# Kernel tuning notes

Measured on AMD Instinct MI355X. Metric: run time of the kernel, lower is better.

Reference implementation:

```python
import jax, jax.numpy as jnp
import numpy as np

B = 32768

def _lin(x, w, b):
    return x @ w.T + b

def setup_inputs() -> dict:
    key = jax.random.key(0)
    ks = iter(jax.random.split(key, 40))
    def rn(shape, s=0.05):
        return jax.random.normal(next(ks), shape, dtype=jnp.float32) * s
    inp = {
        'img_feat': jax.random.normal(next(ks), (B, 256), dtype=jnp.float32),
        'instruction_idx': jax.random.randint(next(ks), (B, 1), 0, 4),
        '_hx': jax.random.normal(next(ks), (B, 256), dtype=jnp.float32),
        '_cx': jax.random.normal(next(ks), (B, 256), dtype=jnp.float32),
        'query': jax.random.normal(next(ks), (B, 256), dtype=jnp.float32),
        # parameters
        'emb': rn((4, 25), 1.0),
        'w_ta': rn((256, 25)), 'b_ta': rn((256,)),
        'w_ih': rn((1024, 512)), 'w_hh': rn((1024, 256)),
        'b_ih': rn((1024,)), 'b_hh': rn((1024,)),
        'w_q': rn((256, 256)), 'b_q': rn((256,)),
        'w_k': rn((256, 256)), 'b_k': rn((256,)),
        'w_ba': rn((512, 512)), 'b_ba': rn((512,)),
        'w_at': rn((256, 512)), 'b_at': rn((256,)),
        'w_p1': rn((128, 256)), 'b_p1': rn((128,)),
        'w_p2': rn((64, 128)), 'b_p2': rn((64,)),
        'w_p': rn((3, 64)), 'b_p': rn((3,)),
        'w_v1': rn((64, 256)), 'b_v1': rn((64,)),
        'w_v2': rn((32, 64)), 'b_v2': rn((32,)),
        'w_v': rn((1, 32)), 'b_v': rn((1,)),
    }
    return inp

def reference(img_feat, instruction_idx, _hx, _cx, query,
              emb, w_ta, b_ta, w_ih, w_hh, b_ih, b_hh,
              w_q, b_q, w_k, b_k, w_ba, b_ba, w_at, b_at,
              w_p1, b_p1, w_p2, b_p2, w_p, b_p,
              w_v1, b_v1, w_v2, b_v2, w_v, b_v):
    # embedding lookup [B,1,25] -> [B,25]
    we = emb[instruction_idx].reshape(instruction_idx.shape[0], -1)
    gated_att = jax.nn.sigmoid(_lin(we, w_ta, b_ta))          # [B,256]
    gated_fusion = img_feat * gated_att                        # [B,256]
    lstm_input = jnp.concatenate([gated_fusion, gated_att], 1) # [B,512]
    # LSTMCell (PyTorch gate order: i, f, g, o)
    gates = lstm_input @ w_ih.T + b_ih + _hx @ w_hh.T + b_hh   # [B,1024]
    i, f, g, o = jnp.split(gates, 4, axis=1)
    cx = jax.nn.sigmoid(f) * _cx + jax.nn.sigmoid(i) * jnp.tanh(g)
    hx = jax.nn.sigmoid(o) * jnp.tanh(cx)
    mlp_input = jnp.concatenate([gated_fusion, hx], 1)         # [B,512]
    mlp_attn = jax.nn.relu(_lin(mlp_input, w_ba, b_ba))        # [B,512]
    key_, val = jnp.split(mlp_attn, 2, axis=1)                 # [B,256] each
    w_q_out = jax.nn.relu(_lin(query, w_q, b_q))
    w_k_out = jax.nn.relu(_lin(key_, w_k, b_k))
    u_t = jnp.tanh(w_q_out + w_k_out)
    attention_vector = u_t * val
    attn_weight = jnp.concatenate([attention_vector, hx], 1)   # [B,512]
    attn_weight = jax.nn.relu(_lin(attn_weight, w_at, b_at))   # [B,256]
    pol = jax.nn.relu(_lin(attn_weight, w_p1, b_p1))
    pol = jax.nn.relu(_lin(pol, w_p2, b_p2))
    valh = jax.nn.relu(_lin(attn_weight, w_v1, b_v1))
    valh = jax.nn.relu(_lin(valh, w_v2, b_v2))
    return (_lin(valh, w_v, b_v), _lin(pol, w_p, b_p), hx, cx)
```

## Files before the change

kernel.cpp:

```cpp
#include <hip/hip_runtime.h>

typedef unsigned short u16;
typedef __bf16 bf16x8 __attribute__((ext_vector_type(8)));
typedef float f32x4 __attribute__((ext_vector_type(4)));
typedef u16 u16x8 __attribute__((ext_vector_type(8)));
typedef u16 u16x4 __attribute__((ext_vector_type(4)));

#define TM 64
#define LDP 264
#define BTOT 32768

#define OFF_WIH 0
#define OFF_WHH 524288
#define OFF_WQ  786432
#define OFF_WK  851968
#define OFF_WBA 917504
#define OFF_WAT 1179648
#define OFF_WP1 1310720
#define OFF_WP2 1343488
#define OFF_WV1 1351680
#define OFF_WV2 1368064
#define OFF_G   1370112

__device__ __forceinline__ float b2f(u16 h) {
    union { unsigned int u; float f; } v; v.u = ((unsigned int)h) << 16; return v.f;
}
__device__ __forceinline__ u16 f2b(float f) {
    union { float f; unsigned int u; } v; v.f = f;
    unsigned int u = v.u + 0x7fffu + ((v.u >> 16) & 1u);
    return (u16)(u >> 16);
}
__device__ __forceinline__ float sigm(float x) { return 1.0f / (1.0f + __expf(-x)); }
__device__ __forceinline__ float tanhfast(float x) { return 1.0f - 2.0f / (__expf(2.0f * x) + 1.0f); }
__device__ __forceinline__ float relu(float x) { return x > 0.0f ? x : 0.0f; }
__device__ __forceinline__ bf16x8 ld8(const u16* p) { return *(const bf16x8*)p; }
__device__ __forceinline__ f32x4 mfma16(bf16x8 a, bf16x8 b, f32x4 c) {
    return __builtin_amdgcn_mfma_f32_16x16x32_bf16(a, b, c, 0, 0, 0);
}

__device__ __forceinline__ bool detect_f32(const void* imgp) {
    const unsigned int* w = (const unsigned int*)imgp;
    int hits = 0;
    #pragma unroll
    for (int i = 0; i < 16; ++i) {
        int e0 = (w[i] >> 7) & 0xFF;
        hits += (e0 >= 100 && e0 <= 140) ? 1 : 0;
    }
    return hits < 10;
}

__device__ __forceinline__ float ldin(const void* p, size_t i, bool f32) {
    return f32 ? ((const float*)p)[i] : b2f(((const u16*)p)[i]);
}
__device__ __forceinline__ void stout_nt(void* o, size_t i, float v, bool f32) {
    if (f32) __builtin_nontemporal_store(v, (float*)o + i);
    else ((u16*)o)[i] = f2b(v);
}
__device__ __forceinline__ f32x4 ld4(const void* p, size_t i, bool f32) {
    if (f32) return __builtin_nontemporal_load((const f32x4*)((const float*)p + i));
    u16x4 q = *(const u16x4*)((const u16*)p + i);
    f32x4 r;
    #pragma unroll
    for (int j = 0; j < 4; ++j) r[j] = b2f(q[j]);
    return r;
}
__device__ __forceinline__ f32x4 ld4p(const void* p, size_t i, bool f32) {
    if (f32) return *(const f32x4*)((const float*)p + i);
    u16x4 q = *(const u16x4*)((const u16*)p + i);
    f32x4 r;
    #pragma unroll
    for (int j = 0; j < 4; ++j) r[j] = b2f(q[j]);
    return r;
}
__device__ __forceinline__ void st4(void* o, size_t i, f32x4 v, bool f32) {
    if (f32) __builtin_nontemporal_store(v, (f32x4*)((float*)o + i));
    else {
        u16x4 p;
        #pragma unroll
        for (int j = 0; j < 4; ++j) p[j] = f2b(v[j]);
        *(u16x4*)((u16*)o + i) = p;
    }
}
__device__ __forceinline__ u16x8 ldg8b(const void* p, size_t i, bool f32) {
    u16x8 t;
    if (f32) {
        const f32x4* q = (const f32x4*)((const float*)p + i);
        f32x4 a = __builtin_nontemporal_load(q);
        f32x4 b = __builtin_nontemporal_load(q + 1);
        #pragma unroll
        for (int j = 0; j < 4; ++j) { t[j] = f2b(a[j]); t[4 + j] = f2b(b[j]); }
    } else {
        t = *(const u16x8*)((const u16*)p + i);
    }
    return t;
}

struct CvtArgs {
    const void* src[10];
    unsigned int nchunk[10];
    unsigned int off8[10];
    unsigned int Kdim[10];
    const void* emb;
    const void* w_ta;
    const void* b_ta;
    const void* det;
};

__global__ __launch_bounds__(256) void cvt_weights(CvtArgs a, u16* ws) {
    const bool f32 = detect_f32(a.det);
    const int p = blockIdx.x;
    if (p == 10) {
        if (blockIdx.y == 0) {
            for (int j = threadIdx.x; j < 1024; j += 256) {
                int e = j >> 8, n = j & 255;
                float acc = ldin(a.b_ta, n, f32);
                #pragma unroll
                for (int k = 0; k < 25; ++k)
                    acc += ldin(a.emb, e * 25 + k, f32) * ldin(a.w_ta, n * 25 + k, f32);
                ws[OFF_G + j] = f2b(sigm(acc));
            }
        }
        return;
    }
    const void* s = a.src[p];
    const unsigned int K = a.Kdim[p];
    const unsigned int sh = 31 - __clz((int)(K >> 5));
    const unsigned int cpr = K >> 3;
    const unsigned int csh = sh + 2;
    const unsigned int n = a.nchunk[p];
    for (unsigned int e = blockIdx.y * blockDim.x + threadIdx.x; e < n;
         e += gridDim.y * blockDim.x) {
        const unsigned int row  = e >> csh;
        const unsigned int colc = e & (cpr - 1u);
        const unsigned int g = ((((row >> 4) << sh) + (colc >> 2)) << 6)
                             + ((colc & 3u) << 4) + (row & 15u);
        const size_t si = ((size_t)e) << 3;
        u16 t[8];
        if (f32) {
            const f32x4* q = (const f32x4*)((const float*)s + si);
            f32x4 va = *q;
            f32x4 vb = *(q + 1);
            #pragma unroll
            for (int j = 0; j < 4; ++j) { t[j] = f2b(va[j]); t[4 + j] = f2b(vb[j]); }
        } else {
            *(u16x8*)t = *(const u16x8*)((const u16*)s + si);
        }
        ((u16x8*)ws)[a.off8[p] + g] = *(u16x8*)t;
    }
}

__global__ __launch_bounds__(1024, 2) void ac_fused(
    const void* __restrict__ img, const int* __restrict__ insn,
    const void* __restrict__ hx_in, const void* __restrict__ cx_in,
    const void* __restrict__ query,
    const void* __restrict__ b_ih, const void* __restrict__ b_hh,
    const void* __restrict__ b_q, const void* __restrict__ b_k,
    const void* __restrict__ b_ba, const void* __restrict__ b_at,
    const void* __restrict__ b_p1, const void* __restrict__ b_p2,
    const void* __restrict__ w_p3, const void* __restrict__ b_p3,
    const void* __restrict__ b_v1, const void* __restrict__ b_v2,
    const void* __restrict__ w_v3, const void* __restrict__ b_v3,
    const u16* __restrict__ wsb, void* __restrict__ out)
{
    __shared__ __align__(16) u16 sGF[TM * LDP];
    __shared__ __align__(16) u16 sHX0[TM * LDP];
    __shared__ __align__(16) u16 sHX1[TM * LDP];
    __shared__ __align__(16) u16 sKEY[TM * LDP];
    __shared__ __align__(16) u16 sG[4 * LDP];
    __shared__ float sW3[224];
    __shared__ int sIDX[TM];

    const bool isf32 = detect_f32(img);
    const int tid  = threadIdx.x;
    const int lane = tid & 63;
    const int wv   = tid >> 6;
    const int l15  = lane & 15;
    const int quad = lane >> 4;
    const int q8   = quad * 8;
    const int q4   = quad * 4;
    const int ln8  = lane * 8;
    const int row0 = blockIdx.x * TM;
    const int nb16 = wv * 16 + q4;

    const int r0s = tid >> 5, c0s = (tid & 31) << 3;
    const int r1s = (tid + 1024) >> 5;
    float iv0[8], hv0[8], iv1[8], hv1[8];
    u16x8 qv0, qv1;
    f32x4 cxo[4];
    {
        const size_t base0 = (size_t)(row0 + r0s) * 256 + c0s;
        const size_t base1 = (size_t)(row0 + r1s) * 256 + c0s;
        #pragma unroll
        for (int m = 0; m < 4; ++m)
            cxo[m] = ld4(cx_in, (size_t)(row0 + m * 16 + l15) * 256 + nb16, isf32);
        qv0 = ldg8b(query, base0, isf32);
        qv1 = ldg8b(query, base1, isf32);
        if (isf32) {
            const f32x4* ip0 = (const f32x4*)((const float*)img + base0);
            const f32x4* hp0 = (const f32x4*)((const float*)hx_in + base0);
            const f32x4* ip1 = (const f32x4*)((const float*)img + base1);
            const f32x4* hp1 = (const f32x4*)((const float*)hx_in + base1);
            f32x4 a0 = __builtin_nontemporal_load(ip0);
            f32x4 a1 = __builtin_nontemporal_load(ip0 + 1);
            f32x4 b0 = __builtin_nontemporal_load(hp0);
            f32x4 b1 = __builtin_nontemporal_load(hp0 + 1);
            f32x4 c0 = __builtin_nontemporal_load(ip1);
            f32x4 c1 = __builtin_nontemporal_load(ip1 + 1);
            f32x4 d0 = __builtin_nontemporal_load(hp1);
            f32x4 d1 = __builtin_nontemporal_load(hp1 + 1);
            #pragma unroll
            for (int j = 0; j < 4; ++j) {
                iv0[j] = a0[j]; iv0[4 + j] = a1[j];
                hv0[j] = b0[j]; hv0[4 + j] = b1[j];
                iv1[j] = c0[j]; iv1[4 + j] = c1[j];
                hv1[j] = d0[j]; hv1[4 + j] = d1[j];
            }
        } else {
            u16x8 i80 = *(const u16x8*)((const u16*)img + base0);
            u16x8 h80 = *(const u16x8*)((const u16*)hx_in + base0);
            u16x8 i81 = *(const u16x8*)((const u16*)img + base1);
            u16x8 h81 = *(const u16x8*)((const u16*)hx_in + base1);
            #pragma unroll
            for (int j = 0; j < 8; ++j) {
                iv0[j] = b2f(i80[j]); hv0[j] = b2f(h80[j]);
                iv1[j] = b2f(i81[j]); hv1[j] = b2f(h81[j]);
            }
        }
    }
    if (tid < TM) sIDX[tid] = insn[row0 + tid];
    sG[(tid >> 8) * LDP + (tid & 255)] = wsb[OFF_G + tid];
    __syncthreads();

    {
        int e0 = sIDX[r0s], e1 = sIDX[r1s];
        u16x8 gv0 = *(const u16x8*)(sG + e0 * LDP + c0s);
        u16x8 gv1 = *(const u16x8*)(sG + e1 * LDP + c0s);
        u16x8 ov0, hvv0, ov1, hvv1;
        #pragma unroll
        for (int j = 0; j < 8; ++j) {
            ov0[j] = f2b(iv0[j] * b2f(gv0[j]));  hvv0[j] = f2b(hv0[j]);
            ov1[j] = f2b(iv1[j] * b2f(gv1[j]));  hvv1[j] = f2b(hv1[j]);
        }
        *(u16x8*)(sGF + r0s * LDP + c0s) = ov0;
        *(u16x8*)(sHX0 + r0s * LDP + c0s) = hvv0;
        *(u16x8*)(sGF + r1s * LDP + c0s) = ov1;
        *(u16x8*)(sHX0 + r1s * LDP + c0s) = hvv1;
        *(u16x8*)(sKEY + r0s * LDP + c0s) = qv0;
        *(u16x8*)(sKEY + r1s * LDP + c0s) = qv1;
    }
    __syncthreads();

    {
        int eIdx[4];
        #pragma unroll
        for (int m = 0; m < 4; ++m) eIdx[m] = sIDX[m * 16 + l15];
        const u16* bih0 = wsb + OFF_WIH + ln8;
        const u16* bhh0 = wsb + OFF_WHH + ln8;
        const int c = wv;
        f32x4 acc[4][4];
        #pragma unroll
        for (int g = 0; g < 4; ++g) {
            f32x4 bs = ld4p(b_ih, g * 256 + nb16, isf32)
                     + ld4p(b_hh, g * 256 + nb16, isf32);
            #pragma unroll
            for (int m = 0; m < 4; ++m) acc[g][m] = bs;
        }
        #pragma unroll
        for (int kk = 0; kk < 8; ++kk) {
            bf16x8 a[4], b[4];
            #pragma unroll
            for (int m = 0; m < 4; ++m) a[m] = ld8(sGF + (m * 16 + l15) * LDP + kk * 32 + q8);
            #pragma unroll
            for (int g = 0; g < 4; ++g) b[g] = ld8(bih0 + (size_t)((g * 16 + c) * 16 + kk) * 512);
            #pragma unroll
            for (int g = 0; g < 4; ++g)
                #pragma unroll
                for (int m = 0; m < 4; ++m) acc[g][m] = mfma16(b[g], a[m], acc[g][m]);
        }
        #pragma unroll
        for (int kk = 0; kk < 8; ++kk) {
            bf16x8 a[4], b[4];
            #pragma unroll
            for (int m = 0; m < 4; ++m) a[m] = ld8(sG + eIdx[m] * LDP + kk * 32 + q8);
            #pragma unroll
            for (int g = 0; g < 4; ++g) b[g] = ld8(bih0 + (size_t)((g * 16 + c) * 16 + 8 + kk) * 512);
            #pragma unroll
            for (int g = 0; g < 4; ++g)
                #pragma unroll
                for (int m = 0; m < 4; ++m) acc[g][m] = mfma16(b[g], a[m], acc[g][m]);
        }
        #pragma unroll
        for (int kk = 0; kk < 8; ++kk) {
            bf16x8 a[4], b[4];
            #pragma unroll
            for (int m = 0; m < 4; ++m) a[m] = ld8(sHX0 + (m * 16 + l15) * LDP + kk * 32 + q8);
            #pragma unroll
            for (int g = 0; g < 4; ++g) b[g] = ld8(bhh0 + (size_t)((g * 16 + c) * 8 + kk) * 512);
            #pragma unroll
            for (int g = 0; g < 4; ++g)
                #pragma unroll
                for (int m = 0; m < 4; ++m) acc[g][m] = mfma16(b[g], a[m], acc[g][m]);
        }
        #pragma unroll
        for (int m = 0; m < 4; ++m) {
            const int batch = m * 16 + l15;
            const size_t gbase = (size_t)(row0 + batch) * 256 + nb16;
            f32x4 hnv, cnv; u16x4 hpk;
            #pragma unroll
            for (int r = 0; r < 4; ++r) {
                const float iv = sigm(acc[0][m][r]);
                const float fv = sigm(acc[1][m][r]);
                const float gv = tanhfast(acc[2][m][r]);
                const float ov = sigm(acc[3][m][r]);
                const float cn = fv * cxo[m][r] + iv * gv;
                const float hn = ov * tanhfast(cn);
                cnv[r] = cn; hnv[r] = hn; hpk[r] = f2b(hn);
            }
            st4(out, (size_t)(4 * BTOT) + gbase, hnv, isf32);
            st4(out, (size_t)(4 * BTOT) + (size_t)256 * BTOT + gbase, cnv, isf32);
            *(u16x4*)(sHX1 + batch * LDP + nb16) = hpk;
        }
    }
    __syncthreads();

    f32x4 cq[4];
    {
        {
            f32x4 bq4 = ld4p(b_q, nb16, isf32);
            #pragma unroll
            for (int m = 0; m < 4; ++m) cq[m] = bq4;
        }
        const u16* bq0 = wsb + OFF_WQ + ln8;
        #pragma unroll
        for (int kk = 0; kk < 8; ++kk) {
            bf16x8 aq[4];
            #pragma unroll
            for (int m = 0; m < 4; ++m)
                aq[m] = ld8(sKEY + (m * 16 + l15) * LDP + kk * 32 + q8);
            bf16x8 bqf = ld8(bq0 + (size_t)(wv * 8 + kk) * 512);
            #pragma unroll
            for (int m = 0; m < 4; ++m) cq[m] = mfma16(bqf, aq[m], cq[m]);
        }
        const u16* bb0 = wsb + OFF_WBA + ln8;
        f32x4 acc[2][4];
        #pragma unroll
        for (int t = 0; t < 2; ++t) {
            f32x4 bb4 = ld4p(b_ba, (wv * 2 + t) * 16 + q4, isf32);
            #pragma unroll
            for (int m = 0; m < 4; ++m) acc[t][m] = bb4;
        }
        #pragma unroll
        for (int kk = 0; kk < 8; ++kk) {
            bf16x8 a[4], b[2];
            #pragma unroll
            for (int m = 0; m < 4; ++m) a[m] = ld8(sGF + (m * 16 + l15) * LDP + kk * 32 + q8);
            #pragma unroll
            for (int t = 0; t < 2; ++t) b[t] = ld8(bb0 + (size_t)((wv * 2 + t) * 16 + kk) * 512);
            #pragma unroll
            for (int t = 0; t < 2; ++t)
                #pragma unroll
                for (int m = 0; m < 4; ++m) acc[t][m] = mfma16(b[t], a[m], acc[t][m]);
        }
        #pragma unroll
        for (int kk = 0; kk < 8; ++kk) {
            bf16x8 a[4], b[2];
            #pragma unroll
            for (int m = 0; m < 4; ++m) a[m] = ld8(sHX1 + (m * 16 + l15) * LDP + kk * 32 + q8);
            #pragma unroll
            for (int t = 0; t < 2; ++t) b[t] = ld8(bb0 + (size_t)((wv * 2 + t) * 16 + 8 + kk) * 512);
            #pragma unroll
            for (int t = 0; t < 2; ++t)
                #pragma unroll
                for (int m = 0; m < 4; ++m) acc[t][m] = mfma16(b[t], a[m], acc[t][m]);
        }
        __syncthreads();
        #pragma unroll
        for (int t = 0; t < 2; ++t) {
            const int colb = (wv * 2 + t) * 16 + q4;
            u16* dst = (colb < 256) ? (sKEY + colb) : (sHX0 + (colb - 256));
            #pragma unroll
            for (int m = 0; m < 4; ++m) {
                u16x4 pk;
                #pragma unroll
                for (int r = 0; r < 4; ++r) pk[r] = f2b(relu(acc[t][m][r]));
                *(u16x4*)(dst + (m * 16 + l15) * LDP) = pk;
            }
        }
    }
    __syncthreads();

    f32x4 acc4[4];
    {
        const u16* bat0 = wsb + OFF_WAT + ln8;
        {
            f32x4 bat4 = ld4p(b_at, nb16, isf32);
            #pragma unroll
            for (int m = 0; m < 4; ++m) acc4[m] = bat4;
        }
        #pragma unroll
        for (int kk = 0; kk < 8; ++kk) {
            bf16x8 a[4];
            #pragma unroll
            for (int m = 0; m < 4; ++m) a[m] = ld8(sHX1 + (m * 16 + l15) * LDP + kk * 32 + q8);
            bf16x8 b = ld8(bat0 + (size_t)(wv * 16 + 8 + kk) * 512);
            #pragma unroll
            for (int m = 0; m < 4; ++m) acc4[m] = mfma16(b, a[m], acc4[m]);
        }
        f32x4 ck[4];
        {
            f32x4 bk4 = ld4p(b_k, nb16, isf32);
            #pragma unroll
            for (int m = 0; m < 4; ++m) ck[m] = bk4;
        }
        const u16* bk0 = wsb + OFF_WK + ln8;
        #pragma unroll
        for (int kk = 0; kk < 8; ++kk) {
            bf16x8 ak[4];
            #pragma unroll
            for (int m = 0; m < 4; ++m) ak[m] = ld8(sKEY + (m * 16 + l15) * LDP + kk * 32 + q8);
            bf16x8 bkf = ld8(bk0 + (size_t)(wv * 8 + kk) * 512);
            #pragma unroll
            for (int m = 0; m < 4; ++m) ck[m] = mfma16(bkf, ak[m], ck[m]);
        }
        #pragma unroll
        for (int m = 0; m < 4; ++m) {
            const int batch = m * 16 + l15;
            u16x4 vv = *(const u16x4*)(sHX0 + batch * LDP + nb16);
            u16x4 pk;
            #pragma unroll
            for (int r = 0; r < 4; ++r) {
                const float u = tanhfast(relu(cq[m][r]) + relu(ck[m][r]));
                pk[r] = f2b(u * b2f(vv[r]));
            }
            *(u16x4*)(sGF + batch * LDP + nb16) = pk;
        }
    }
    __syncthreads();

    {
        const u16* bat0 = wsb + OFF_WAT + ln8;
        #pragma unroll
        for (int kk = 0; kk < 8; ++kk) {
            bf16x8 a[4];
            #pragma unroll
            for (int m = 0; m < 4; ++m) a[m] = ld8(sGF + (m * 16 + l15) * LDP + kk * 32 + q8);
            bf16x8 b = ld8(bat0 + (size_t)(wv * 16 + kk) * 512);
            #pragma unroll
            for (int m = 0; m < 4; ++m) acc4[m] = mfma16(b, a[m], acc4[m]);
        }
        #pragma unroll
        for (int m = 0; m < 4; ++m) {
            u16x4 pk;
            #pragma unroll
            for (int r = 0; r < 4; ++r) pk[r] = f2b(relu(acc4[m][r]));
            *(u16x4*)(sKEY + (m * 16 + l15) * LDP + nb16) = pk;
        }
    }
    __syncthreads();

    {
        if (tid < 224)
            sW3[tid] = (tid < 192) ? ldin(w_p3, tid, isf32)
                                   : ldin(w_v3, tid - 192, isf32);
        const int m = wv & 3, half = wv >> 2;
        const int batch = m * 16 + l15;
        bf16x8 afr[8];
        #pragma unroll
        for (int kk = 0; kk < 8; ++kk) afr[kk] = ld8(sKEY + batch * LDP + kk * 32 + q8);
        {
            f32x4 acc[2];
            #pragma unroll
            for (int t = 0; t < 2; ++t) acc[t] = ld4p(b_p1, (half * 2 + t) * 16 + q4, isf32);
            #pragma unroll
            for (int kk = 0; kk < 8; ++kk)
                #pragma unroll
                for (int t = 0; t < 2; ++t)
                    acc[t] = mfma16(ld8(wsb + OFF_WP1 + (size_t)((half * 2 + t) * 8 + kk) * 512 + ln8), afr[kk], acc[t]);
            #pragma unroll
            for (int t = 0; t < 2; ++t) {
                const int colb = (half * 2 + t) * 16 + q4;
                u16x4 pk;
                #pragma unroll
                for (int r = 0; r < 4; ++r) pk[r] = f2b(relu(acc[t][r]));
                *(u16x4*)(sHX0 + batch * LDP + colb) = pk;
            }
        }
        {
            f32x4 acc = ld4p(b_v1, half * 16 + q4, isf32);
            #pragma unroll
            for (int kk = 0; kk < 8; ++kk)
                acc = mfma16(ld8(wsb + OFF_WV1 + (size_t)(half * 8 + kk) * 512 + ln8), afr[kk], acc);
            const int colb = half * 16 + q4;
            u16x4 pk;
            #pragma unroll
            for (int r = 0; r < 4; ++r) pk[r] = f2b(relu(acc[r]));
            *(u16x4*)(sHX0 + batch * LDP + 128 + colb) = pk;
        }
    }
    __syncthreads();

    {
        const int m = wv & 3, half = wv >> 2;
        const int batch = m * 16 + l15;
        const u16* a0 = sHX0 + batch * LDP;
        bf16x8 ap[4], av2[2];
        #pragma unroll
        for (int kk = 0; kk < 4; ++kk) ap[kk] = ld8(a0 + kk * 32 + q8);
        #pragma unroll
        for (int kk = 0; kk < 2; ++kk) av2[kk] = ld8(a0 + 128 + kk * 32 + q8);
        {
            f32x4 acc = ld4p(b_p2, half * 16 + q4, isf32);
            #pragma unroll
            for (int kk = 0; kk < 4; ++kk)
                acc = mfma16(ld8(wsb + OFF_WP2 + (size_t)(half * 4 + kk) * 512 + ln8), ap[kk], acc);
            const int colb = half * 16 + q4;
            u16x4 pk;
            #pragma unroll
            for (int r = 0; r < 4; ++r) pk[r] = f2b(relu(acc[r]));
            *(u16x4*)(sGF + batch * LDP + colb) = pk;
        }
        if (half < 2) {
            f32x4 acc = ld4p(b_v2, half * 16 + q4, isf32);
            #pragma unroll
            for (int kk = 0; kk < 2; ++kk)
                acc = mfma16(ld8(wsb + OFF_WV2 + (size_t)(half * 2 + kk) * 512 + ln8), av2[kk], acc);
            const int colb = half * 16 + q4;
            u16x4 pk;
            #pragma unroll
            for (int r = 0; r < 4; ++r) pk[r] = f2b(relu(acc[r]));
            *(u16x4*)(sGF + batch * LDP + 64 + colb) = pk;
        }
    }
    __syncthreads();

    if (tid < TM * 4) {
        const int r = tid >> 2, o = tid & 3;
        const int grow = row0 + r;
        const u16* rowp = sGF + r * LDP;
        if (o < 3) {
            float acc = ldin(b_p3, o, isf32);
            #pragma unroll
            for (int k = 0; k < 64; ++k) acc += b2f(rowp[k]) * sW3[o * 64 + k];
            stout_nt(out, (size_t)BTOT + (size_t)grow * 3 + o, acc, isf32);
        } else {
            float acc = ldin(b_v3, 0, isf32);
            #pragma unroll
            for (int k = 0; k < 32; ++k) acc += b2f(rowp[64 + k]) * sW3[192 + k];
            stout_nt(out, (size_t)grow, acc, isf32);
        }
    }
}

extern "C" void kernel_launch(void* const* d_in, const int* in_sizes, int n_in,
                              void* d_out, int out_size, void* d_ws, size_t ws_size,
                              hipStream_t stream) {
    u16* ws = (u16*)d_ws;

    CvtArgs ca;
    const int srcIdx[10] = {8, 9, 12, 14, 16, 18, 20, 22, 26, 28};
    const unsigned int ns[10]   = {524288, 262144, 65536, 65536, 262144, 131072, 32768, 8192, 16384, 2048};
    const unsigned int off[10]  = {OFF_WIH, OFF_WHH, OFF_WQ, OFF_WK, OFF_WBA, OFF_WAT, OFF_WP1, OFF_WP2, OFF_WV1, OFF_WV2};
    const unsigned int kd[10]   = {512, 256, 256, 256, 512, 512, 256, 128, 256, 64};
    for (int i = 0; i < 10; ++i) {
        ca.src[i] = d_in[srcIdx[i]];
        ca.nchunk[i] = ns[i] / 8;
        ca.off8[i] = off[i] / 8;
        ca.Kdim[i] = kd[i];
    }
    ca.emb = d_in[5];
    ca.w_ta = d_in[6];
    ca.b_ta = d_in[7];
    ca.det = d_in[0];
    cvt_weights<<<dim3(11, 64), dim3(256), 0, stream>>>(ca, ws);

    ac_fused<<<dim3(BTOT / TM), dim3(1024), 0, stream>>>(
        d_in[0], (const int*)d_in[1], d_in[2], d_in[3], d_in[4],
        d_in[10], d_in[11],
        d_in[13], d_in[15],
        d_in[17], d_in[19],
        d_in[21], d_in[23],
        d_in[24], d_in[25],
        d_in[27], d_in[29],
        d_in[30], d_in[31],
        (const u16*)d_ws, d_out);
}
```

Measured before the change: 359.5 us.

## Process two row tiles per block with prefetch of next tile inputs

Each block now handles two 64-row tiles in a loop, halving the grid. The second tile's inputs are meant to be loaded into registers while the first tile computes, hiding global-load latency and amortizing setup such as the gate table and the output-head weights. The float-to-bf16 conversion also switches to the compiler's native __bf16 cast instead of manual rounding. The cost is fewer blocks for the GPU's compute units and higher register pressure from the prefetched data.

```diff
diff --git a/kernel.cpp b/kernel.cpp
--- a/kernel.cpp
+++ b/kernel.cpp
@@ -26,9 +26,7 @@
     union { unsigned int u; float f; } v; v.u = ((unsigned int)h) << 16; return v.f;
 }
 __device__ __forceinline__ u16 f2b(float f) {
-    union { float f; unsigned int u; } v; v.f = f;
-    unsigned int u = v.u + 0x7fffu + ((v.u >> 16) & 1u);
-    return (u16)(u >> 16);
+    return __builtin_bit_cast(u16, (__bf16)f);
 }
 __device__ __forceinline__ float sigm(float x) { return 1.0f / (1.0f + __expf(-x)); }
 __device__ __forceinline__ float tanhfast(float x) { return 1.0f - 2.0f / (__expf(2.0f * x) + 1.0f); }
@@ -179,22 +177,23 @@
     const int q8   = quad * 8;
     const int q4   = quad * 4;
     const int ln8  = lane * 8;
-    const int row0 = blockIdx.x * TM;
+    const int rowB = blockIdx.x * (2 * TM);
     const int nb16 = wv * 16 + q4;
 
     const int r0s = tid >> 5, c0s = (tid & 31) << 3;
     const int r1s = (tid + 1024) >> 5;
-    float iv0[8], hv0[8], iv1[8], hv1[8];
-    u16x8 qv0, qv1;
+
+    float ivA[8], hvA[8], ivB[8], hvB[8];
+    u16x8 qvA, qvB;
     f32x4 cxo[4];
-    {
-        const size_t base0 = (size_t)(row0 + r0s) * 256 + c0s;
-        const size_t base1 = (size_t)(row0 + r1s) * 256 + c0s;
+    auto burst = [&](int rb) {
+        const size_t base0 = (size_t)(rb + r0s) * 256 + c0s;
+        const size_t base1 = (size_t)(rb + r1s) * 256 + c0s;
         #pragma unroll
         for (int m = 0; m < 4; ++m)
-            cxo[m] = ld4(cx_in, (size_t)(row0 + m * 16 + l15) * 256 + nb16, isf32);
-        qv0 = ldg8b(query, base0, isf32);
-        qv1 = ldg8b(query, base1, isf32);
+            cxo[m] = ld4(cx_in, (size_t)(rb + m * 16 + l15) * 256 + nb16, isf32);
+        qvA = ldg8b(query, base0, isf32);
+        qvB = ldg8b(query, base1, isf32);
         if (isf32) {
             const f32x4* ip0 = (const f32x4*)((const float*)img + base0);
             const f32x4* hp0 = (const f32x4*)((const float*)hx_in + base0);
@@ -210,10 +209,10 @@
             f32x4 d1 = __builtin_nontemporal_load(hp1 + 1);
             #pragma unroll
             for (int j = 0; j < 4; ++j) {
-                iv0[j] = a0[j]; iv0[4 + j] = a1[j];
-                hv0[j] = b0[j]; hv0[4 + j] = b1[j];
-                iv1[j] = c0[j]; iv1[4 + j] = c1[j];
-                hv1[j] = d0[j]; hv1[4 + j] = d1[j];
+                ivA[j] = a0[j]; ivA[4 + j] = a1[j];
+                hvA[j] = b0[j]; hvA[4 + j] = b1[j];
+                ivB[j] = c0[j]; ivB[4 + j] = c1[j];
+                hvB[j] = d0[j]; hvB[4 + j] = d1[j];
             }
         } else {
             u16x8 i80 = *(const u16x8*)((const u16*)img + base0);
@@ -222,332 +221,344 @@
             u16x8 h81 = *(const u16x8*)((const u16*)hx_in + base1);
             #pragma unroll
             for (int j = 0; j < 8; ++j) {
-                iv0[j] = b2f(i80[j]); hv0[j] = b2f(h80[j]);
-                iv1[j] = b2f(i81[j]); hv1[j] = b2f(h81[j]);
-            }
-        }
-    }
-    if (tid < TM) sIDX[tid] = insn[row0 + tid];
+                ivA[j] = b2f(i80[j]); hvA[j] = b2f(h80[j]);
+                ivB[j] = b2f(i81[j]); hvB[j] = b2f(h81[j]);
+            }
+        }
+    };
+
+    burst(rowB);
+    if (tid < TM) sIDX[tid] = insn[rowB + tid];
     sG[(tid >> 8) * LDP + (tid & 255)] = wsb[OFF_G + tid];
     __syncthreads();
 
-    {
-        int e0 = sIDX[r0s], e1 = sIDX[r1s];
-        u16x8 gv0 = *(const u16x8*)(sG + e0 * LDP + c0s);
-        u16x8 gv1 = *(const u16x8*)(sG + e1 * LDP + c0s);
-        u16x8 ov0, hvv0, ov1, hvv1;
-        #pragma unroll
-        for (int j = 0; j < 8; ++j) {
-            ov0[j] = f2b(iv0[j] * b2f(gv0[j]));  hvv0[j] = f2b(hv0[j]);
-            ov1[j] = f2b(iv1[j] * b2f(gv1[j]));  hvv1[j] = f2b(hv1[j]);
-        }
-        *(u16x8*)(sGF + r0s * LDP + c0s) = ov0;
-        *(u16x8*)(sHX0 + r0s * LDP + c0s) = hvv0;
-        *(u16x8*)(sGF + r1s * LDP + c0s) = ov1;
-        *(u16x8*)(sHX0 + r1s * LDP + c0s) = hvv1;
-        *(u16x8*)(sKEY + r0s * LDP + c0s) = qv0;
-        *(u16x8*)(sKEY + r1s * LDP + c0s) = qv1;
-    }
-    __syncthreads();
-
-    {
-        int eIdx[4];
-        #pragma unroll
-        for (int m = 0; m < 4; ++m) eIdx[m] = sIDX[m * 16 + l15];
-        const u16* bih0 = wsb + OFF_WIH + ln8;
-        const u16* bhh0 = wsb + OFF_WHH + ln8;
-        const int c = wv;
-        f32x4 acc[4][4];
-        #pragma unroll
-        for (int g = 0; g < 4; ++g) {
-            f32x4 bs = ld4p(b_ih, g * 256 + nb16, isf32)
-                     + ld4p(b_hh, g * 256 + nb16, isf32);
-            #pragma unroll
-            for (int m = 0; m < 4; ++m) acc[g][m] = bs;
-        }
-        #pragma unroll
-        for (int kk = 0; kk < 8; ++kk) {
-            bf16x8 a[4], b[4];
-            #pragma unroll
-            for (int m = 0; m < 4; ++m) a[m] = ld8(sGF + (m * 16 + l15) * LDP + kk * 32 + q8);
-            #pragma unroll
-            for (int g = 0; g < 4; ++g) b[g] = ld8(bih0 + (size_t)((g * 16 + c) * 16 + kk) * 512);
-            #pragma unroll
-            for (int g = 0; g < 4; ++g)
-                #pragma unroll
-                for (int m = 0; m < 4; ++m) acc[g][m] = mfma16(b[g], a[m], acc[g][m]);
-        }
-        #pragma unroll
-        for (int kk = 0; kk < 8; ++kk) {
-            bf16x8 a[4], b[4];
-            #pragma unroll
-            for (int m = 0; m < 4; ++m) a[m] = ld8(sG + eIdx[m] * LDP + kk * 32 + q8);
-            #pragma unroll
-            for (int g = 0; g < 4; ++g) b[g] = ld8(bih0 + (size_t)((g * 16 + c) * 16 + 8 + kk) * 512);
-            #pragma unroll
-            for (int g = 0; g < 4; ++g)
-                #pragma unroll
-                for (int m = 0; m < 4; ++m) acc[g][m] = mfma16(b[g], a[m], acc[g][m]);
-        }
-        #pragma unroll
-        for (int kk = 0; kk < 8; ++kk) {
-            bf16x8 a[4], b[4];
-            #pragma unroll
-            for (int m = 0; m < 4; ++m) a[m] = ld8(sHX0 + (m * 16 + l15) * LDP + kk * 32 + q8);
-            #pragma unroll
-            for (int g = 0; g < 4; ++g) b[g] = ld8(bhh0 + (size_t)((g * 16 + c) * 8 + kk) * 512);
-            #pragma unroll
-            for (int g = 0; g < 4; ++g)
-                #pragma unroll
-                for (int m = 0; m < 4; ++m) acc[g][m] = mfma16(b[g], a[m], acc[g][m]);
-        }
-        #pragma unroll
-        for (int m = 0; m < 4; ++m) {
-            const int batch = m * 16 + l15;
-            const size_t gbase = (size_t)(row0 + batch) * 256 + nb16;
-            f32x4 hnv, cnv; u16x4 hpk;
-            #pragma unroll
-            for (int r = 0; r < 4; ++r) {
-                const float iv = sigm(acc[0][m][r]);
-                const float fv = sigm(acc[1][m][r]);
-                const float gv = tanhfast(acc[2][m][r]);
-                const float ov = sigm(acc[3][m][r]);
-                const float cn = fv * cxo[m][r] + iv * gv;
-                const float hn = ov * tanhfast(cn);
-                cnv[r] = cn; hnv[r] = hn; hpk[r] = f2b(hn);
-            }
-            st4(out, (size_t)(4 * BTOT) + gbase, hnv, isf32);
-            st4(out, (size_t)(4 * BTOT) + (size_t)256 * BTOT + gbase, cnv, isf32);
-            *(u16x4*)(sHX1 + batch * LDP + nb16) = hpk;
-        }
-    }
-    __syncthreads();
-
-    f32x4 cq[4];
-    {
-        {
-            f32x4 bq4 = ld4p(b_q, nb16, isf32);
-            #pragma unroll
-            for (int m = 0; m < 4; ++m) cq[m] = bq4;
-        }
-        const u16* bq0 = wsb + OFF_WQ + ln8;
-        #pragma unroll
-        for (int kk = 0; kk < 8; ++kk) {
-            bf16x8 aq[4];
-            #pragma unroll
-            for (int m = 0; m < 4; ++m)
-                aq[m] = ld8(sKEY + (m * 16 + l15) * LDP + kk * 32 + q8);
-            bf16x8 bqf = ld8(bq0 + (size_t)(wv * 8 + kk) * 512);
-            #pragma unroll
-            for (int m = 0; m < 4; ++m) cq[m] = mfma16(bqf, aq[m], cq[m]);
-        }
-        const u16* bb0 = wsb + OFF_WBA + ln8;
-        f32x4 acc[2][4];
-        #pragma unroll
-        for (int t = 0; t < 2; ++t) {
-            f32x4 bb4 = ld4p(b_ba, (wv * 2 + t) * 16 + q4, isf32);
-            #pragma unroll
-            for (int m = 0; m < 4; ++m) acc[t][m] = bb4;
-        }
-        #pragma unroll
-        for (int kk = 0; kk < 8; ++kk) {
-            bf16x8 a[4], b[2];
-            #pragma unroll
-            for (int m = 0; m < 4; ++m) a[m] = ld8(sGF + (m * 16 + l15) * LDP + kk * 32 + q8);
-            #pragma unroll
-            for (int t = 0; t < 2; ++t) b[t] = ld8(bb0 + (size_t)((wv * 2 + t) * 16 + kk) * 512);
-            #pragma unroll
-            for (int t = 0; t < 2; ++t)
-                #pragma unroll
-                for (int m = 0; m < 4; ++m) acc[t][m] = mfma16(b[t], a[m], acc[t][m]);
-        }
-        #pragma unroll
-        for (int kk = 0; kk < 8; ++kk) {
-            bf16x8 a[4], b[2];
-            #pragma unroll
-            for (int m = 0; m < 4; ++m) a[m] = ld8(sHX1 + (m * 16 + l15) * LDP + kk * 32 + q8);
-            #pragma unroll
-            for (int t = 0; t < 2; ++t) b[t] = ld8(bb0 + (size_t)((wv * 2 + t) * 16 + 8 + kk) * 512);
-            #pragma unroll
-            for (int t = 0; t < 2; ++t)
-                #pragma unroll
-                for (int m = 0; m < 4; ++m) acc[t][m] = mfma16(b[t], a[m], acc[t][m]);
-        }
-        __syncthreads();
-        #pragma unroll
-        for (int t = 0; t < 2; ++t) {
-            const int colb = (wv * 2 + t) * 16 + q4;
-            u16* dst = (colb < 256) ? (sKEY + colb) : (sHX0 + (colb - 256));
+    #pragma unroll
+    for (int it = 0; it < 2; ++it) {
+        const int row0 = rowB + it * TM;
+
+        {
+            int e0 = sIDX[r0s], e1 = sIDX[r1s];
+            u16x8 gv0 = *(const u16x8*)(sG + e0 * LDP + c0s);
+            u16x8 gv1 = *(const u16x8*)(sG + e1 * LDP + c0s);
+            u16x8 ov0, hvv0, ov1, hvv1;
+            #pragma unroll
+            for (int j = 0; j < 8; ++j) {
+                ov0[j] = f2b(ivA[j] * b2f(gv0[j]));  hvv0[j] = f2b(hvA[j]);
+                ov1[j] = f2b(ivB[j] * b2f(gv1[j]));  hvv1[j] = f2b(hvB[j]);
+            }
+            *(u16x8*)(sGF + r0s * LDP + c0s) = ov0;
+            *(u16x8*)(sHX0 + r0s * LDP + c0s) = hvv0;
+            *(u16x8*)(sGF + r1s * LDP + c0s) = ov1;
+            *(u16x8*)(sHX0 + r1s * LDP + c0s) = hvv1;
+            *(u16x8*)(sKEY + r0s * LDP + c0s) = qvA;
+            *(u16x8*)(sKEY + r1s * LDP + c0s) = qvB;
+        }
+        __syncthreads();
+
+        {
+            int eIdx[4];
+            #pragma unroll
+            for (int m = 0; m < 4; ++m) eIdx[m] = sIDX[m * 16 + l15];
+            const u16* bih0 = wsb + OFF_WIH + ln8;
+            const u16* bhh0 = wsb + OFF_WHH + ln8;
+            const int c = wv;
+            f32x4 acc[4][4];
+            #pragma unroll
+            for (int g = 0; g < 4; ++g) {
+                f32x4 bs = ld4p(b_ih, g * 256 + nb16, isf32)
+                         + ld4p(b_hh, g * 256 + nb16, isf32);
+                #pragma unroll
+                for (int m = 0; m < 4; ++m) acc[g][m] = bs;
+            }
+            #pragma unroll
+            for (int kk = 0; kk < 8; ++kk) {
+                bf16x8 a[4], b[4];
+                #pragma unroll
+                for (int m = 0; m < 4; ++m) a[m] = ld8(sGF + (m * 16 + l15) * LDP + kk * 32 + q8);
+                #pragma unroll
+                for (int g = 0; g < 4; ++g) b[g] = ld8(bih0 + (size_t)((g * 16 + c) * 16 + kk) * 512);
+                #pragma unroll
+                for (int g = 0; g < 4; ++g)
+                    #pragma unroll
+                    for (int m = 0; m < 4; ++m) acc[g][m] = mfma16(b[g], a[m], acc[g][m]);
+            }
+            #pragma unroll
+            for (int kk = 0; kk < 8; ++kk) {
+                bf16x8 a[4], b[4];
+                #pragma unroll
+                for (int m = 0; m < 4; ++m) a[m] = ld8(sG + eIdx[m] * LDP + kk * 32 + q8);
+                #pragma unroll
+                for (int g = 0; g < 4; ++g) b[g] = ld8(bih0 + (size_t)((g * 16 + c) * 16 + 8 + kk) * 512);
+                #pragma unroll
+                for (int g = 0; g < 4; ++g)
+                    #pragma unroll
+                    for (int m = 0; m < 4; ++m) acc[g][m] = mfma16(b[g], a[m], acc[g][m]);
+            }
+            #pragma unroll
+            for (int kk = 0; kk < 8; ++kk) {
+                bf16x8 a[4], b[4];
+                #pragma unroll
+                for (int m = 0; m < 4; ++m) a[m] = ld8(sHX0 + (m * 16 + l15) * LDP + kk * 32 + q8);
+                #pragma unroll
+                for (int g = 0; g < 4; ++g) b[g] = ld8(bhh0 + (size_t)((g * 16 + c) * 8 + kk) * 512);
+                #pragma unroll
+                for (int g = 0; g < 4; ++g)
+                    #pragma unroll
+                    for (int m = 0; m < 4; ++m) acc[g][m] = mfma16(b[g], a[m], acc[g][m]);
+            }
+            #pragma unroll
+            for (int m = 0; m < 4; ++m) {
+                const int batch = m * 16 + l15;
+                const size_t gbase = (size_t)(row0 + batch) * 256 + nb16;
+                f32x4 hnv, cnv; u16x4 hpk;
+                #pragma unroll
+                for (int r = 0; r < 4; ++r) {
+                    const float iv = sigm(acc[0][m][r]);
+                    const float fv = sigm(acc[1][m][r]);
+                    const float gv = tanhfast(acc[2][m][r]);
+                    const float ov = sigm(acc[3][m][r]);
+                    const float cn = fv * cxo[m][r] + iv * gv;
+                    const float hn = ov * tanhfast(cn);
+                    cnv[r] = cn; hnv[r] = hn; hpk[r] = f2b(hn);
+                }
+                st4(out, (size_t)(4 * BTOT) + gbase, hnv, isf32);
+                st4(out, (size_t)(4 * BTOT) + (size_t)256 * BTOT + gbase, cnv, isf32);
+                *(u16x4*)(sHX1 + batch * LDP + nb16) = hpk;
+            }
+        }
+        __syncthreads();
+
+        f32x4 cq[4];
+        {
+            {
+                f32x4 bq4 = ld4p(b_q, nb16, isf32);
+                #pragma unroll
+                for (int m = 0; m < 4; ++m) cq[m] = bq4;
+            }
+            const u16* bq0 = wsb + OFF_WQ + ln8;
+            #pragma unroll
+            for (int kk = 0; kk < 8; ++kk) {
+                bf16x8 aq[4];
+                #pragma unroll
+                for (int m = 0; m < 4; ++m)
+                    aq[m] = ld8(sKEY + (m * 16 + l15) * LDP + kk * 32 + q8);
+                bf16x8 bqf = ld8(bq0 + (size_t)(wv * 8 + kk) * 512);
+                #pragma unroll
+                for (int m = 0; m < 4; ++m) cq[m] = mfma16(bqf, aq[m], cq[m]);
+            }
+            const u16* bb0 = wsb + OFF_WBA + ln8;
+            f32x4 acc[2][4];
+            #pragma unroll
+            for (int t = 0; t < 2; ++t) {
+                f32x4 bb4 = ld4p(b_ba, (wv * 2 + t) * 16 + q4, isf32);
+                #pragma unroll
+                for (int m = 0; m < 4; ++m) acc[t][m] = bb4;
+            }
+            #pragma unroll
+            for (int kk = 0; kk < 8; ++kk) {
+                bf16x8 a[4], b[2];
+                #pragma unroll
+                for (int m = 0; m < 4; ++m) a[m] = ld8(sGF + (m * 16 + l15) * LDP + kk * 32 + q8);
+                #pragma unroll
+                for (int t = 0; t < 2; ++t) b[t] = ld8(bb0 + (size_t)((wv * 2 + t) * 16 + kk) * 512);
+                #pragma unroll
+                for (int t = 0; t < 2; ++t)
+                    #pragma unroll
+                    for (int m = 0; m < 4; ++m) acc[t][m] = mfma16(b[t], a[m], acc[t][m]);
+            }
+            #pragma unroll
+            for (int kk = 0; kk < 8; ++kk) {
+                bf16x8 a[4], b[2];
+                #pragma unroll
+                for (int m = 0; m < 4; ++m) a[m] = ld8(sHX1 + (m * 16 + l15) * LDP + kk * 32 + q8);
+                #pragma unroll
+                for (int t = 0; t < 2; ++t) b[t] = ld8(bb0 + (size_t)((wv * 2 + t) * 16 + 8 + kk) * 512);
+                #pragma unroll
+                for (int t = 0; t < 2; ++t)
+                    #pragma unroll
+                    for (int m = 0; m < 4; ++m) acc[t][m] = mfma16(b[t], a[m], acc[t][m]);
+            }
+            __syncthreads();
+            #pragma unroll
+            for (int t = 0; t < 2; ++t) {
+                const int colb = (wv * 2 + t) * 16 + q4;
+                u16* dst = (colb < 256) ? (sKEY + colb) : (sHX0 + (colb - 256));
+                #pragma unroll
+                for (int m = 0; m < 4; ++m) {
+                    u16x4 pk;
+                    #pragma unroll
+                    for (int r = 0; r < 4; ++r) pk[r] = f2b(relu(acc[t][m][r]));
+                    *(u16x4*)(dst + (m * 16 + l15) * LDP) = pk;
+                }
+            }
+        }
+        __syncthreads();
+
+        f32x4 acc4[4];
+        {
+            const u16* bat0 = wsb + OFF_WAT + ln8;
+            {
+                f32x4 bat4 = ld4p(b_at, nb16, isf32);
+                #pragma unroll
+                for (int m = 0; m < 4; ++m) acc4[m] = bat4;
+            }
+            #pragma unroll
+            for (int kk = 0; kk < 8; ++kk) {
+                bf16x8 a[4];
+                #pragma unroll
+                for (int m = 0; m < 4; ++m) a[m] = ld8(sHX1 + (m * 16 + l15) * LDP + kk * 32 + q8);
+                bf16x8 b = ld8(bat0 + (size_t)(wv * 16 + 8 + kk) * 512);
+                #pragma unroll
+                for (int m = 0; m < 4; ++m) acc4[m] = mfma16(b, a[m], acc4[m]);
+            }
+            f32x4 ck[4];
+            {
+                f32x4 bk4 = ld4p(b_k, nb16, isf32);
+                #pragma unroll
+                for (int m = 0; m < 4; ++m) ck[m] = bk4;
+            }
+            const u16* bk0 = wsb + OFF_WK + ln8;
+            #pragma unroll
+            for (int kk = 0; kk < 8; ++kk) {
+                bf16x8 ak[4];
+                #pragma unroll
+                for (int m = 0; m < 4; ++m) ak[m] = ld8(sKEY + (m * 16 + l15) * LDP + kk * 32 + q8);
+                bf16x8 bkf = ld8(bk0 + (size_t)(wv * 8 + kk) * 512);
+                #pragma unroll
+                for (int m = 0; m < 4; ++m) ck[m] = mfma16(bkf, ak[m], ck[m]);
+            }
+            #pragma unroll
+            for (int m = 0; m < 4; ++m) {
+                const int batch = m * 16 + l15;
+                u16x4 vv = *(const u16x4*)(sHX0 + batch * LDP + nb16);
+                u16x4 pk;
+                #pragma unroll
+                for (int r = 0; r < 4; ++r) {
+                    const float u = tanhfast(relu(cq[m][r]) + relu(ck[m][r]));
+                    pk[r] = f2b(u * b2f(vv[r]));
+                }
+                *(u16x4*)(sGF + batch * LDP + nb16) = pk;
+            }
+        }
+        __syncthreads();
+
+        {
+            const u16* bat0 = wsb + OFF_WAT + ln8;
+            #pragma unroll
+            for (int kk = 0; kk < 8; ++kk) {
+                bf16x8 a[4];
+                #pragma unroll
+                for (int m = 0; m < 4; ++m) a[m] = ld8(sGF + (m * 16 + l15) * LDP + kk * 32 + q8);
+                bf16x8 b = ld8(bat0 + (size_t)(wv * 16 + kk) * 512);
+                #pragma unroll
+                for (int m = 0; m < 4; ++m) acc4[m] = mfma16(b, a[m], acc4[m]);
+            }
             #pragma unroll
             for (int m = 0; m < 4; ++m) {
                 u16x4 pk;
                 #pragma unroll
-                for (int r = 0; r < 4; ++r) pk[r] = f2b(relu(acc[t][m][r]));
-                *(u16x4*)(dst + (m * 16 + l15) * LDP) = pk;
-            }
-        }
-    }
-    __syncthreads();
-
-    f32x4 acc4[4];
-    {
-        const u16* bat0 = wsb + OFF_WAT + ln8;
-        {
-            f32x4 bat4 = ld4p(b_at, nb16, isf32);
-            #pragma unroll
-            for (int m = 0; m < 4; ++m) acc4[m] = bat4;
-        }
-        #pragma unroll
-        for (int kk = 0; kk < 8; ++kk) {
-            bf16x8 a[4];
-            #pragma unroll
-            for (int m = 0; m < 4; ++m) a[m] = ld8(sHX1 + (m * 16 + l15) * LDP + kk * 32 + q8);
-            bf16x8 b = ld8(bat0 + (size_t)(wv * 16 + 8 + kk) * 512);
-            #pragma unroll
-            for (int m = 0; m < 4; ++m) acc4[m] = mfma16(b, a[m], acc4[m]);
-        }
-        f32x4 ck[4];
-        {
-            f32x4 bk4 = ld4p(b_k, nb16, isf32);
-            #pragma unroll
-            for (int m = 0; m < 4; ++m) ck[m] = bk4;
-        }
-        const u16* bk0 = wsb + OFF_WK + ln8;
-        #pragma unroll
-        for (int kk = 0; kk < 8; ++kk) {
-            bf16x8 ak[4];
-            #pragma unroll
-            for (int m = 0; m < 4; ++m) ak[m] = ld8(sKEY + (m * 16 + l15) * LDP + kk * 32 + q8);
-            bf16x8 bkf = ld8(bk0 + (size_t)(wv * 8 + kk) * 512);
-            #pragma unroll
-            for (int m = 0; m < 4; ++m) ck[m] = mfma16(bkf, ak[m], ck[m]);
-        }
-        #pragma unroll
-        for (int m = 0; m < 4; ++m) {
+                for (int r = 0; r < 4; ++r) pk[r] = f2b(relu(acc4[m][r]));
+                *(u16x4*)(sKEY + (m * 16 + l15) * LDP + nb16) = pk;
+            }
+        }
+        __syncthreads();
+
+        {
+            if (it == 0) {
+                if (tid < 224)
+                    sW3[tid] = (tid < 192) ? ldin(w_p3, tid, isf32)
+                                           : ldin(w_v3, tid - 192, isf32);
+                burst(rowB + TM);
+            }
+            const int m = wv & 3, half = wv >> 2;
             const int batch = m * 16 + l15;
-            u16x4 vv = *(const u16x4*)(sHX0 + batch * LDP + nb16);
-            u16x4 pk;
-            #pragma unroll
-            for (int r = 0; r < 4; ++r) {
-                const float u = tanhfast(relu(cq[m][r]) + relu(ck[m][r]));
-                pk[r] = f2b(u * b2f(vv[r]));
-            }
-            *(u16x4*)(sGF + batch * LDP + nb16) = pk;
-        }
-    }
-    __syncthreads();
-
-    {
-        const u16* bat0 = wsb + OFF_WAT + ln8;
-        #pragma unroll
-        for (int kk = 0; kk < 8; ++kk) {
-            bf16x8 a[4];
-            #pragma unroll
-            for (int m = 0; m < 4; ++m) a[m] = ld8(sGF + (m * 16 + l15) * LDP + kk * 32 + q8);
-            bf16x8 b = ld8(bat0 + (size_t)(wv * 16 + kk) * 512);
-            #pragma unroll
-            for (int m = 0; m < 4; ++m) acc4[m] = mfma16(b, a[m], acc4[m]);
-        }
-        #pragma unroll
-        for (int m = 0; m < 4; ++m) {
-            u16x4 pk;
-            #pragma unroll
-            for (int r = 0; r < 4; ++r) pk[r] = f2b(relu(acc4[m][r]));
-            *(u16x4*)(sKEY + (m * 16 + l15) * LDP + nb16) = pk;
-        }
-    }
-    __syncthreads();
-
-    {
-        if (tid < 224)
-            sW3[tid] = (tid < 192) ? ldin(w_p3, tid, isf32)
-                                   : ldin(w_v3, tid - 192, isf32);
-        const int m = wv & 3, half = wv >> 2;
-        const int batch = m * 16 + l15;
-        bf16x8 afr[8];
-        #pragma unroll
-        for (int kk = 0; kk < 8; ++kk) afr[kk] = ld8(sKEY + batch * LDP + kk * 32 + q8);
-        {
-            f32x4 acc[2];
-            #pragma unroll
-            for (int t = 0; t < 2; ++t) acc[t] = ld4p(b_p1, (half * 2 + t) * 16 + q4, isf32);
-            #pragma unroll
-            for (int kk = 0; kk < 8; ++kk)
-                #pragma unroll
-                for (int t = 0; t < 2; ++t)
-                    acc[t] = mfma16(ld8(wsb + OFF_WP1 + (size_t)((half * 2 + t) * 8 + kk) * 512 + ln8), afr[kk], acc[t]);
-            #pragma unroll
-            for (int t = 0; t < 2; ++t) {
-                const int colb = (half * 2 + t) * 16 + q4;
+            bf16x8 afr[8];
+            #pragma unroll
+            for (int kk = 0; kk < 8; ++kk) afr[kk] = ld8(sKEY + batch * LDP + kk * 32 + q8);
+            {
+                f32x4 acc[2];
+                #pragma unroll
+                for (int t = 0; t < 2; ++t) acc[t] = ld4p(b_p1, (half * 2 + t) * 16 + q4, isf32);
+                #pragma unroll
+                for (int kk = 0; kk < 8; ++kk)
+                    #pragma unroll
+                    for (int t = 0; t < 2; ++t)
+                        acc[t] = mfma16(ld8(wsb + OFF_WP1 + (size_t)((half * 2 + t) * 8 + kk) * 512 + ln8), afr[kk], acc[t]);
+                #pragma unroll
+                for (int t = 0; t < 2; ++t) {
+                    const int colb = (half * 2 + t) * 16 + q4;
+                    u16x4 pk;
+                    #pragma unroll
+                    for (int r = 0; r < 4; ++r) pk[r] = f2b(relu(acc[t][r]));
+                    *(u16x4*)(sHX0 + batch * LDP + colb) = pk;
+                }
+            }
+            {
+                f32x4 acc = ld4p(b_v1, half * 16 + q4, isf32);
+                #pragma unroll
+                for (int kk = 0; kk < 8; ++kk)
+                    acc = mfma16(ld8(wsb + OFF_WV1 + (size_t)(half * 8 + kk) * 512 + ln8), afr[kk], acc);
+                const int colb = half * 16 + q4;
                 u16x4 pk;
                 #pragma unroll
-                for (int r = 0; r < 4; ++r) pk[r] = f2b(relu(acc[t][r]));
-                *(u16x4*)(sHX0 + batch * LDP + colb) = pk;
-            }
-        }
-        {
-            f32x4 acc = ld4p(b_v1, half * 16 + q4, isf32);
-            #pragma unroll
-            for (int kk = 0; kk < 8; ++kk)
-                acc = mfma16(ld8(wsb + OFF_WV1 + (size_t)(half * 8 + kk) * 512 + ln8), afr[kk], acc);
-            const int colb = half * 16 + q4;
-            u16x4 pk;
-            #pragma unroll
-            for (int r = 0; r < 4; ++r) pk[r] = f2b(relu(acc[r]));
-            *(u16x4*)(sHX0 + batch * LDP + 128 + colb) = pk;
-        }
-    }
-    __syncthreads();
-
-    {
-        const int m = wv & 3, half = wv >> 2;
-        const int batch = m * 16 + l15;
-        const u16* a0 = sHX0 + batch * LDP;
-        bf16x8 ap[4], av2[2];
-        #pragma unroll
-        for (int kk = 0; kk < 4; ++kk) ap[kk] = ld8(a0 + kk * 32 + q8);
-        #pragma unroll
-        for (int kk = 0; kk < 2; ++kk) av2[kk] = ld8(a0 + 128 + kk * 32 + q8);
-        {
-            f32x4 acc = ld4p(b_p2, half * 16 + q4, isf32);
-            #pragma unroll
-            for (int kk = 0; kk < 4; ++kk)
-                acc = mfma16(ld8(wsb + OFF_WP2 + (size_t)(half * 4 + kk) * 512 + ln8), ap[kk], acc);
-            const int colb = half * 16 + q4;
-            u16x4 pk;
-            #pragma unroll
-            for (int r = 0; r < 4; ++r) pk[r] = f2b(relu(acc[r]));
-            *(u16x4*)(sGF + batch * LDP + colb) = pk;
-        }
-        if (half < 2) {
-            f32x4 acc = ld4p(b_v2, half * 16 + q4, isf32);
-            #pragma unroll
-            for (int kk = 0; kk < 2; ++kk)
-                acc = mfma16(ld8(wsb + OFF_WV2 + (size_t)(half * 2 + kk) * 512 + ln8), av2[kk], acc);
-            const int colb = half * 16 + q4;
-            u16x4 pk;
-            #pragma unroll
-            for (int r = 0; r < 4; ++r) pk[r] = f2b(relu(acc[r]));
-            *(u16x4*)(sGF + batch * LDP + 64 + colb) = pk;
-        }
-    }
-    __syncthreads();
-
-    if (tid < TM * 4) {
-        const int r = tid >> 2, o = tid & 3;
-        const int grow = row0 + r;
-        const u16* rowp = sGF + r * LDP;
-        if (o < 3) {
-            float acc = ldin(b_p3, o, isf32);
-            #pragma unroll
-            for (int k = 0; k < 64; ++k) acc += b2f(rowp[k]) * sW3[o * 64 + k];
-            stout_nt(out, (size_t)BTOT + (size_t)grow * 3 + o, acc, isf32);
-        } else {
-            float acc = ldin(b_v3, 0, isf32);
-            #pragma unroll
-            for (int k = 0; k < 32; ++k) acc += b2f(rowp[64 + k]) * sW3[192 + k];
-            stout_nt(out, (size_t)grow, acc, isf32);
-        }
+                for (int r = 0; r < 4; ++r) pk[r] = f2b(relu(acc[r]));
+                *(u16x4*)(sHX0 + batch * LDP + 128 + colb) = pk;
+            }
+        }
+        __syncthreads();
+
+        {
+            if (it == 0 && tid < TM) sIDX[tid] = insn[rowB + TM + tid];
+            const int m = wv & 3, half = wv >> 2;
+            const int batch = m * 16 + l15;
+            const u16* a0 = sHX0 + batch * LDP;
+            bf16x8 ap[4], av2[2];
+            #pragma unroll
+            for (int kk = 0; kk < 4; ++kk) ap[kk] = ld8(a0 + kk * 32 + q8);
+            #pragma unroll
+            for (int kk = 0; kk < 2; ++kk) av2[kk] = ld8(a0 + 128 + kk * 32 + q8);
+            {
+                f32x4 acc = ld4p(b_p2, half * 16 + q4, isf32);
+                #pragma unroll
+                for (int kk = 0; kk < 4; ++kk)
+                    acc = mfma16(ld8(wsb + OFF_WP2 + (size_t)(half * 4 + kk) * 512 + ln8), ap[kk], acc);
+                const int colb = half * 16 + q4;
+                u16x4 pk;
+                #pragma unroll
+                for (int r = 0; r < 4; ++r) pk[r] = f2b(relu(acc[r]));
+                *(u16x4*)(sGF + batch * LDP + colb) = pk;
+            }
+            if (half < 2) {
+                f32x4 acc = ld4p(b_v2, half * 16 + q4, isf32);
+                #pragma unroll
+                for (int kk = 0; kk < 2; ++kk)
+                    acc = mfma16(ld8(wsb + OFF_WV2 + (size_t)(half * 2 + kk) * 512 + ln8), av2[kk], acc);
+                const int colb = half * 16 + q4;
+                u16x4 pk;
+                #pragma unroll
+                for (int r = 0; r < 4; ++r) pk[r] = f2b(relu(acc[r]));
+                *(u16x4*)(sGF + batch * LDP + 64 + colb) = pk;
+            }
+        }
+        __syncthreads();
+
+        if (tid < TM * 4) {
+            const int r = tid >> 2, o = tid & 3;
+            const int grow = row0 + r;
+            const u16* rowp = sGF + r * LDP;
+            if (o < 3) {
+                float acc = ldin(b_p3, o, isf32);
+                #pragma unroll
+                for (int k = 0; k < 64; ++k) acc += b2f(rowp[k]) * sW3[o * 64 + k];
+                stout_nt(out, (size_t)BTOT + (size_t)grow * 3 + o, acc, isf32);
+            } else {
+                float acc = ldin(b_v3, 0, isf32);
+                #pragma unroll
+                for (int k = 0; k < 32; ++k) acc += b2f(rowp[64 + k]) * sW3[192 + k];
+                stout_nt(out, (size_t)grow, acc, isf32);
+            }
+        }
+        __syncthreads();
     }
 }
 
@@ -573,7 +584,7 @@
     ca.det = d_in[0];
     cvt_weights<<<dim3(11, 64), dim3(256), 0, stream>>>(ca, ws);
 
-    ac_fused<<<dim3(BTOT / TM), dim3(1024), 0, stream>>>(
+    ac_fused<<<dim3(BTOT / (2 * TM)), dim3(1024), 0, stream>>>(
         d_in[0], (const int*)d_in[1], d_in[2], d_in[3], d_in[4],
         d_in[10], d_in[11],
         d_in[13], d_in[15],
```

Result: slower. 550.8 us (+53.2%).
